# Kernel optimization log

Measured on AMD Instinct MI355X. Metric: run time of the kernel, lower is better.

Reference implementation:

```python
import jax, jax.numpy as jnp
import numpy as np

D_K = 64
D_MODEL = 1024
N_HEADS = 16


def setup_inputs() -> dict:
    key = jax.random.key(0)
    ks = jax.random.split(key, 9)
    B, S = 2, 2048
    scale = 1.0 / np.sqrt(D_MODEL)
    inp = {
        "x": jax.random.normal(ks[0], (B, S, D_MODEL), dtype=jnp.float32),
        "w_q": jax.random.normal(ks[1], (D_MODEL, N_HEADS * D_K), dtype=jnp.float32) * scale,
        "b_q": jnp.zeros((N_HEADS * D_K,), dtype=jnp.float32),
        "w_k": jax.random.normal(ks[2], (D_MODEL, N_HEADS * D_K), dtype=jnp.float32) * scale,
        "b_k": jnp.zeros((N_HEADS * D_K,), dtype=jnp.float32),
        "w_v": jax.random.normal(ks[3], (D_MODEL, N_HEADS * D_K), dtype=jnp.float32) * scale,
        "b_v": jnp.zeros((N_HEADS * D_K,), dtype=jnp.float32),
        "w_o": jax.random.normal(ks[4], (N_HEADS * D_K, D_MODEL), dtype=jnp.float32) * scale,
        "b_o": jnp.zeros((D_MODEL,), dtype=jnp.float32),
    }
    return inp


def reference(x, w_q, b_q, w_k, b_k, w_v, b_v, w_o, b_o):
    B, S, _ = x.shape
    H, Dk = N_HEADS, D_K

    def split_heads(m):  # [B,S,H*Dk] -> [B,H,S,Dk]
        return m.reshape(B, S, H, Dk).transpose(0, 2, 1, 3)

    Q = split_heads(x @ w_q + b_q)
    K = split_heads(x @ w_k + b_k)
    V = split_heads(x @ w_v + b_v)

    scores = jnp.einsum("bhsd,bhtd->bhst", Q, K) / jnp.sqrt(jnp.float32(Dk))
    probs = jax.nn.softmax(scores, axis=-1)
    attn = jnp.einsum("bhst,bhtd->bhsd", probs, V)  # [B,H,S,Dk]
    attn = attn.transpose(0, 2, 1, 3).reshape(B, S, H * Dk)
    return attn @ w_o + b_o
```

## Files before the change

### kernel.cpp

```cpp
#include <hip/hip_runtime.h>
#include <math.h>

#define D_MODELc 1024
#define N_HEADSc 16
#define D_Kc     64
#define B_SZc    2
#define S_LENc   2048
#define NTOKc    (B_SZc * S_LENc)

using half8  = __attribute__((ext_vector_type(8))) _Float16;
using half4  = __attribute__((ext_vector_type(4))) _Float16;
using float4v = __attribute__((ext_vector_type(4))) float;

__global__ __launch_bounds__(256) void cvt_all(
    const float* __restrict__ x,
    const float* __restrict__ W0, const float* __restrict__ W1,
    const float* __restrict__ W2, const float* __restrict__ W3,
    _Float16* __restrict__ wout, _Float16* __restrict__ xout)
{
    __shared__ float T[32][33];
    const int z = blockIdx.z;
    const int t = threadIdx.x;

    if (z == 4) {
        const int bid = blockIdx.y * 32 + blockIdx.x;
        #pragma unroll
        for (int c = 0; c < 2; ++c) {
            const int i = bid * 512 + c * 256 + t;
            float4v a = ((const float4v*)x)[2 * i];
            float4v b = ((const float4v*)x)[2 * i + 1];
            half8 h;
            h[0] = (_Float16)a[0]; h[1] = (_Float16)a[1];
            h[2] = (_Float16)a[2]; h[3] = (_Float16)a[3];
            h[4] = (_Float16)b[0]; h[5] = (_Float16)b[1];
            h[6] = (_Float16)b[2]; h[7] = (_Float16)b[3];
            ((half8*)xout)[i] = h;
        }
        return;
    }

    const float* W = (z == 0) ? W0 : (z == 1) ? W1 : (z == 2) ? W2 : W3;
    _Float16* O = wout + (size_t)z * 1024 * 1024;

    const int k0 = blockIdx.x * 32;
    const int n0 = blockIdx.y * 32;
    {
        const int r = t >> 3, c4 = (t & 7) * 4;
        float4v v = *(const float4v*)(W + (size_t)(k0 + r) * 1024 + n0 + c4);
        T[r][c4 + 0] = v[0]; T[r][c4 + 1] = v[1];
        T[r][c4 + 2] = v[2]; T[r][c4 + 3] = v[3];
    }
    __syncthreads();
    {
        const int rn = t >> 3, ck4 = (t & 7) * 4;
        half4 h;
        h[0] = (_Float16)T[ck4 + 0][rn];
        h[1] = (_Float16)T[ck4 + 1][rn];
        h[2] = (_Float16)T[ck4 + 2][rn];
        h[3] = (_Float16)T[ck4 + 3][rn];
        *(half4*)(O + (size_t)(n0 + rn) * 1024 + k0 + ck4) = h;
    }
}

template <int MODE>
__global__ __launch_bounds__(256) void gemm_f16(
    const _Float16* __restrict__ A, const _Float16* __restrict__ BtAll,
    const float* __restrict__ bias0, const float* __restrict__ bias1,
    const float* __restrict__ bias2, void* __restrict__ Cout)
{
    __shared__ _Float16 Als[128 * 32];
    __shared__ _Float16 Bls[128 * 32];

    constexpr int K = 1024;
    const int tid = threadIdx.x;
    const int m0  = blockIdx.x * 128;
    const int n0  = blockIdx.y * 128;
    const int z   = blockIdx.z;

    const _Float16* Bt  = BtAll + (size_t)z * 1024 * 1024;
    const float* bias   = (z == 0) ? bias0 : (z == 1) ? bias1 : bias2;
    const float qscale  = (MODE == 1 && z == 0) ? 0.18033688011112042f : 1.0f;

    const int wave = tid >> 6, lane = tid & 63;
    const int wr = wave >> 1, wc = wave & 1;
    const int quad = lane >> 4, l16 = lane & 15;

    float4v acc[4][4];
    #pragma unroll
    for (int i = 0; i < 4; ++i)
        #pragma unroll
        for (int j = 0; j < 4; ++j)
            acc[i][j] = (float4v){0.f, 0.f, 0.f, 0.f};

    for (int k0 = 0; k0 < K; k0 += 32) {
        #pragma unroll
        for (int c = 0; c < 2; ++c) {
            const int i   = c * 256 + tid;
            const int row = i >> 2, kc = i & 3;
            const _Float16* ga = A  + (size_t)(m0 + row) * K + k0 + kc * 8;
            const _Float16* gb = Bt + (size_t)(n0 + row) * K + k0 + kc * 8;
            __builtin_amdgcn_global_load_lds(
                (const __attribute__((address_space(1))) void*)ga,
                (__attribute__((address_space(3))) void*)(Als + i * 8), 16, 0, 0);
            __builtin_amdgcn_global_load_lds(
                (const __attribute__((address_space(1))) void*)gb,
                (__attribute__((address_space(3))) void*)(Bls + i * 8), 16, 0, 0);
        }
        __syncthreads();

        half8 af[4], bf[4];
        #pragma unroll
        for (int i = 0; i < 4; ++i) {
            const int r = wr * 64 + i * 16 + l16;
            af[i] = *(const half8*)(Als + r * 32 + quad * 8);
        }
        #pragma unroll
        for (int j = 0; j < 4; ++j) {
            const int cidx = wc * 64 + j * 16 + l16;
            bf[j] = *(const half8*)(Bls + cidx * 32 + quad * 8);
        }
        #pragma unroll
        for (int i = 0; i < 4; ++i)
            #pragma unroll
            for (int j = 0; j < 4; ++j)
                acc[i][j] = __builtin_amdgcn_mfma_f32_16x16x32_f16(
                    af[i], bf[j], acc[i][j], 0, 0, 0);
        __syncthreads();
    }

    if constexpr (MODE == 0) {
        #pragma unroll
        for (int i = 0; i < 4; ++i) {
            const int rbase = m0 + wr * 64 + i * 16 + quad * 4;
            #pragma unroll
            for (int j = 0; j < 4; ++j) {
                const int col = n0 + wc * 64 + j * 16 + l16;
                const float bv = bias[col];
                #pragma unroll
                for (int r = 0; r < 4; ++r)
                    ((float*)Cout)[(size_t)(rbase + r) * 1024 + col] =
                        acc[i][j][r] + bv;
            }
        }
    } else {
        if (z != 2) {
            #pragma unroll
            for (int i = 0; i < 4; ++i) {
                const int rbase = m0 + wr * 64 + i * 16 + quad * 4;
                #pragma unroll
                for (int j = 0; j < 4; ++j) {
                    const int col = n0 + wc * 64 + j * 16 + l16;
                    const float bv = bias[col];
                    #pragma unroll
                    for (int r = 0; r < 4; ++r) {
                        const float v = (acc[i][j][r] + bv) * qscale;
                        const int n = rbase + r;
                        const int b = n >> 11, s = n & 2047;
                        const int h = col >> 6, d = col & 63;
                        _Float16* C = (_Float16*)Cout + (size_t)z * NTOKc * D_MODELc;
                        C[(((size_t)(b * N_HEADSc + h)) * S_LENc + s) * D_Kc + d] =
                            (_Float16)v;
                    }
                }
            }
        } else {
            __shared__ _Float16 Tb[4 * 64 * 72];
            _Float16* tb = Tb + wave * (64 * 72);
            #pragma unroll
            for (int i = 0; i < 4; ++i) {
                #pragma unroll
                for (int j = 0; j < 4; ++j) {
                    const int col = n0 + wc * 64 + j * 16 + l16;
                    const float bv = bias[col];
                    half4 hv;
                    #pragma unroll
                    for (int r = 0; r < 4; ++r)
                        hv[r] = (_Float16)(acc[i][j][r] + bv);
                    *(half4*)(tb + (j * 16 + l16) * 72 + i * 16 + quad * 4) = hv;
                }
            }
            const int hh   = (n0 >> 6) + wc;
            const int tok0 = m0 + wr * 64;
            const int bb   = tok0 >> 11, sb = tok0 & 2047;
            const int dl   = lane >> 3, t8 = (lane & 7) * 8;
            _Float16* Vout = (_Float16*)Cout + (size_t)2 * NTOKc * D_MODELc;
            #pragma unroll
            for (int p = 0; p < 8; ++p) {
                const int d = p * 8 + dl;
                half8 hv = *(const half8*)(tb + d * 72 + t8);
                *(half8*)(Vout +
                    (((size_t)(bb * N_HEADSc + hh)) * D_Kc + d) * S_LENc +
                    sb + t8) = hv;
            }
        }
    }
}

__global__ __launch_bounds__(256) void attn_mfma(
    const _Float16* __restrict__ Qb, const _Float16* __restrict__ Kb,
    const _Float16* __restrict__ Vtg, _Float16* __restrict__ Ab)
{
    constexpr int PS = 72;
    __shared__ _Float16 Ks[64 * PS];
    __shared__ _Float16 Vt[64 * PS];
    __shared__ _Float16 Ps[128 * PS];
    __shared__ float    Al[128];

    const int tid  = threadIdx.x;
    const int wv   = tid >> 6;
    const int lane = tid & 63;
    const int quad = lane >> 4;
    const int l16  = lane & 15;

    const int q0 = blockIdx.x * 128;
    const int bh = blockIdx.y;
    const int b  = bh >> 4, h = bh & 15;

    const _Float16* Qsl = Qb  + (size_t)bh * S_LENc * D_Kc;
    const _Float16* Ksl = Kb  + (size_t)bh * S_LENc * D_Kc;
    const _Float16* Vsl = Vtg + (size_t)bh * S_LENc * D_Kc;

    half8 aq[2][2];
    #pragma unroll
    for (int qf = 0; qf < 2; ++qf) {
        const int row = q0 + wv * 32 + qf * 16 + l16;
        aq[qf][0] = *(const half8*)(Qsl + (size_t)row * 64 + quad * 8);
        aq[qf][1] = *(const half8*)(Qsl + (size_t)row * 64 + 32 + quad * 8);
    }

    float4v O[2][4];
    #pragma unroll
    for (int qf = 0; qf < 2; ++qf)
        #pragma unroll
        for (int nt = 0; nt < 4; ++nt)
            O[qf][nt] = (float4v){0.f, 0.f, 0.f, 0.f};
    float lr[2] = {0.f, 0.f};

    const int sr = tid >> 2;
    const int sg = (tid & 3) * 16;

    for (int t0 = 0; t0 < S_LENc; t0 += 64) {
        half8 k0 = *(const half8*)(Ksl + (size_t)(t0 + sr) * 64 + sg);
        half8 k1 = *(const half8*)(Ksl + (size_t)(t0 + sr) * 64 + sg + 8);
        half8 v0 = *(const half8*)(Vsl + (size_t)sr * S_LENc + t0 + sg);
        half8 v1 = *(const half8*)(Vsl + (size_t)sr * S_LENc + t0 + sg + 8);
        __syncthreads();
        *(half8*)(Ks + sr * PS + sg)     = k0;
        *(half8*)(Ks + sr * PS + sg + 8) = k1;
        *(half8*)(Vt + sr * PS + sg)     = v0;
        *(half8*)(Vt + sr * PS + sg + 8) = v1;
        __syncthreads();

        half8 kf[4][2];
        #pragma unroll
        for (int nt = 0; nt < 4; ++nt) {
            kf[nt][0] = *(const half8*)(Ks + (nt * 16 + l16) * PS + quad * 8);
            kf[nt][1] = *(const half8*)(Ks + (nt * 16 + l16) * PS + 32 + quad * 8);
        }

        #pragma unroll
        for (int qf = 0; qf < 2; ++qf) {
            float4v st[4];
            #pragma unroll
            for (int nt = 0; nt < 4; ++nt) {
                st[nt] = __builtin_amdgcn_mfma_f32_16x16x32_f16(
                    kf[nt][0], aq[qf][0], (float4v){0.f, 0.f, 0.f, 0.f}, 0, 0, 0);
                st[nt] = __builtin_amdgcn_mfma_f32_16x16x32_f16(
                    kf[nt][1], aq[qf][1], st[nt], 0, 0, 0);
            }
            float ls = 0.f;
            #pragma unroll
            for (int nt = 0; nt < 4; ++nt) {
                half4 pk;
                #pragma unroll
                for (int r = 0; r < 4; ++r) {
                    const float p = exp2f(fminf(st[nt][r], 15.5f));
                    ls += p;
                    pk[r] = (_Float16)p;
                }
                *(half4*)(Ps + (wv * 32 + qf * 16 + l16) * PS +
                          nt * 16 + quad * 4) = pk;
            }
            lr[qf] += ls;
        }

        half8 bvv[4][2];
        #pragma unroll
        for (int nt = 0; nt < 4; ++nt) {
            bvv[nt][0] = *(const half8*)(Vt + (nt * 16 + l16) * PS + quad * 8);
            bvv[nt][1] = *(const half8*)(Vt + (nt * 16 + l16) * PS + 32 + quad * 8);
        }
        #pragma unroll
        for (int qf = 0; qf < 2; ++qf) {
            half8 ap0 = *(const half8*)(Ps + (wv * 32 + qf * 16 + l16) * PS + quad * 8);
            half8 ap1 = *(const half8*)(Ps + (wv * 32 + qf * 16 + l16) * PS + 32 + quad * 8);
            #pragma unroll
            for (int nt = 0; nt < 4; ++nt) {
                O[qf][nt] = __builtin_amdgcn_mfma_f32_16x16x32_f16(
                    ap0, bvv[nt][0], O[qf][nt], 0, 0, 0);
                O[qf][nt] = __builtin_amdgcn_mfma_f32_16x16x32_f16(
                    ap1, bvv[nt][1], O[qf][nt], 0, 0, 0);
            }
        }
    }

    #pragma unroll
    for (int qf = 0; qf < 2; ++qf) {
        float t = lr[qf];
        t += __shfl_xor(t, 16, 64);
        t += __shfl_xor(t, 32, 64);
        if (quad == 0) Al[wv * 32 + qf * 16 + l16] = 1.0f / t;
    }
    #pragma unroll
    for (int qf = 0; qf < 2; ++qf) {
        float4v iv = *(const float4v*)(Al + wv * 32 + qf * 16 + quad * 4);
        #pragma unroll
        for (int r = 0; r < 4; ++r) {
            const int q = q0 + wv * 32 + qf * 16 + quad * 4 + r;
            _Float16* dst = Ab + ((size_t)(b * S_LENc + q)) * 1024 + h * 64;
            #pragma unroll
            for (int nt = 0; nt < 4; ++nt)
                dst[nt * 16 + l16] = (_Float16)(O[qf][nt][r] * iv[r]);
        }
    }
}

extern "C" void kernel_launch(void* const* d_in, const int* in_sizes, int n_in,
                              void* d_out, int out_size, void* d_ws, size_t ws_size,
                              hipStream_t stream)
{
    const float* x  = (const float*)d_in[0];
    const float* wq = (const float*)d_in[1];
    const float* bq = (const float*)d_in[2];
    const float* wk = (const float*)d_in[3];
    const float* bk = (const float*)d_in[4];
    const float* wv = (const float*)d_in[5];
    const float* bv = (const float*)d_in[6];
    const float* wo = (const float*)d_in[7];
    const float* bo = (const float*)d_in[8];
    float* out = (float*)d_out;

    const size_t M1 = 1024 * 1024;
    const size_t M4 = 4 * M1;
    _Float16* xh = (_Float16*)d_ws;
    _Float16* wh = xh + M4;
    _Float16* Qh = wh + M4;
    _Float16* Ah = Qh + 3 * M4;

    cvt_all<<<dim3(32, 32, 5), dim3(256), 0, stream>>>(
        x, wq, wk, wv, wo, wh, xh);
    gemm_f16<1><<<dim3(NTOKc / 128, D_MODELc / 128, 3), dim3(256), 0, stream>>>(
        xh, wh, bq, bk, bv, Qh);
    attn_mfma<<<dim3(S_LENc / 128, B_SZc * N_HEADSc), dim3(256), 0, stream>>>(
        Qh, Qh + M4, Qh + 2 * M4, Ah);
    gemm_f16<0><<<dim3(NTOKc / 128, D_MODELc / 128, 1), dim3(256), 0, stream>>>(
        Ah, wh + 3 * M1, bo, bo, bo, out);
}
```

Baseline: 216.6 us.

## Split attention over key halves with a combine kernel, simplify V store

```diff
diff --git a/kernel.cpp b/kernel.cpp
--- a/kernel.cpp
+++ b/kernel.cpp
@@ -10,6 +10,7 @@
 
 using half8  = __attribute__((ext_vector_type(8))) _Float16;
 using half4  = __attribute__((ext_vector_type(4))) _Float16;
+using fp16x2 = __attribute__((ext_vector_type(2))) __fp16;
 using float4v = __attribute__((ext_vector_type(4))) float;
 
 __global__ __launch_bounds__(256) void cvt_all(
@@ -164,33 +165,23 @@
                 }
             }
         } else {
-            __shared__ _Float16 Tb[4 * 64 * 72];
-            _Float16* tb = Tb + wave * (64 * 72);
             #pragma unroll
             for (int i = 0; i < 4; ++i) {
+                const int rbase = m0 + wr * 64 + i * 16 + quad * 4;
+                const int b = rbase >> 11, s0 = rbase & 2047;
                 #pragma unroll
                 for (int j = 0; j < 4; ++j) {
                     const int col = n0 + wc * 64 + j * 16 + l16;
                     const float bv = bias[col];
+                    const int h = col >> 6, d = col & 63;
                     half4 hv;
                     #pragma unroll
                     for (int r = 0; r < 4; ++r)
                         hv[r] = (_Float16)(acc[i][j][r] + bv);
-                    *(half4*)(tb + (j * 16 + l16) * 72 + i * 16 + quad * 4) = hv;
+                    _Float16* C = (_Float16*)Cout + (size_t)2 * NTOKc * D_MODELc;
+                    *(half4*)(C + (((size_t)(b * N_HEADSc + h)) * D_Kc + d) *
+                              S_LENc + s0) = hv;
                 }
-            }
-            const int hh   = (n0 >> 6) + wc;
-            const int tok0 = m0 + wr * 64;
-            const int bb   = tok0 >> 11, sb = tok0 & 2047;
-            const int dl   = lane >> 3, t8 = (lane & 7) * 8;
-            _Float16* Vout = (_Float16*)Cout + (size_t)2 * NTOKc * D_MODELc;
-            #pragma unroll
-            for (int p = 0; p < 8; ++p) {
-                const int d = p * 8 + dl;
-                half8 hv = *(const half8*)(tb + d * 72 + t8);
-                *(half8*)(Vout +
-                    (((size_t)(bb * N_HEADSc + hh)) * D_Kc + d) * S_LENc +
-                    sb + t8) = hv;
             }
         }
     }
@@ -198,13 +189,13 @@
 
 __global__ __launch_bounds__(256) void attn_mfma(
     const _Float16* __restrict__ Qb, const _Float16* __restrict__ Kb,
-    const _Float16* __restrict__ Vtg, _Float16* __restrict__ Ab)
+    const _Float16* __restrict__ Vtg, _Float16* __restrict__ Op,
+    float* __restrict__ Lp)
 {
     constexpr int PS = 72;
     __shared__ _Float16 Ks[64 * PS];
     __shared__ _Float16 Vt[64 * PS];
     __shared__ _Float16 Ps[128 * PS];
-    __shared__ float    Al[128];
 
     const int tid  = threadIdx.x;
     const int wv   = tid >> 6;
@@ -214,7 +205,8 @@
 
     const int q0 = blockIdx.x * 128;
     const int bh = blockIdx.y;
-    const int b  = bh >> 4, h = bh & 15;
+    const int sp = blockIdx.z;
+    const int kb = sp * (S_LENc / 2);
 
     const _Float16* Qsl = Qb  + (size_t)bh * S_LENc * D_Kc;
     const _Float16* Ksl = Kb  + (size_t)bh * S_LENc * D_Kc;
@@ -239,7 +231,7 @@
     const int sr = tid >> 2;
     const int sg = (tid & 3) * 16;
 
-    for (int t0 = 0; t0 < S_LENc; t0 += 64) {
+    for (int t0 = kb; t0 < kb + S_LENc / 2; t0 += 64) {
         half8 k0 = *(const half8*)(Ksl + (size_t)(t0 + sr) * 64 + sg);
         half8 k1 = *(const half8*)(Ksl + (size_t)(t0 + sr) * 64 + sg + 8);
         half8 v0 = *(const half8*)(Vsl + (size_t)sr * S_LENc + t0 + sg);
@@ -271,15 +263,16 @@
             float ls = 0.f;
             #pragma unroll
             for (int nt = 0; nt < 4; ++nt) {
-                half4 pk;
-                #pragma unroll
-                for (int r = 0; r < 4; ++r) {
-                    const float p = exp2f(fminf(st[nt][r], 15.5f));
-                    ls += p;
-                    pk[r] = (_Float16)p;
-                }
+                const float p0 = __builtin_amdgcn_exp2f(fminf(st[nt][0], 15.5f));
+                const float p1 = __builtin_amdgcn_exp2f(fminf(st[nt][1], 15.5f));
+                const float p2 = __builtin_amdgcn_exp2f(fminf(st[nt][2], 15.5f));
+                const float p3 = __builtin_amdgcn_exp2f(fminf(st[nt][3], 15.5f));
+                ls += (p0 + p1) + (p2 + p3);
+                union { fp16x2 h2[2]; half4 h4; } u;
+                u.h2[0] = __builtin_amdgcn_cvt_pkrtz(p0, p1);
+                u.h2[1] = __builtin_amdgcn_cvt_pkrtz(p2, p3);
                 *(half4*)(Ps + (wv * 32 + qf * 16 + l16) * PS +
-                          nt * 16 + quad * 4) = pk;
+                          nt * 16 + quad * 4) = u.h4;
             }
             lr[qf] += ls;
         }
@@ -304,25 +297,44 @@
         }
     }
 
+    const size_t qgb = (size_t)bh * S_LENc;
     #pragma unroll
     for (int qf = 0; qf < 2; ++qf) {
         float t = lr[qf];
         t += __shfl_xor(t, 16, 64);
         t += __shfl_xor(t, 32, 64);
-        if (quad == 0) Al[wv * 32 + qf * 16 + l16] = 1.0f / t;
-    }
-    #pragma unroll
-    for (int qf = 0; qf < 2; ++qf) {
-        float4v iv = *(const float4v*)(Al + wv * 32 + qf * 16 + quad * 4);
+        if (quad == 0)
+            Lp[(size_t)sp * 65536 + qgb + q0 + wv * 32 + qf * 16 + l16] = t;
         #pragma unroll
         for (int r = 0; r < 4; ++r) {
             const int q = q0 + wv * 32 + qf * 16 + quad * 4 + r;
-            _Float16* dst = Ab + ((size_t)(b * S_LENc + q)) * 1024 + h * 64;
+            _Float16* dst = Op + ((size_t)sp * 65536 + qgb + q) * 64;
             #pragma unroll
             for (int nt = 0; nt < 4; ++nt)
-                dst[nt * 16 + l16] = (_Float16)(O[qf][nt][r] * iv[r]);
-        }
-    }
+                dst[nt * 16 + l16] = (_Float16)O[qf][nt][r];
+        }
+    }
+}
+
+__global__ __launch_bounds__(256) void attn_combine(
+    const _Float16* __restrict__ Op, const float* __restrict__ Lp,
+    _Float16* __restrict__ Ab)
+{
+    const int i  = blockIdx.x * 256 + threadIdx.x;
+    const int e0 = i * 8;
+    const int qg = e0 >> 6;
+    const int d0 = e0 & 63;
+    const int bh = qg >> 11, q = qg & 2047;
+    const int b  = bh >> 4,  h = bh & 15;
+
+    const float inv = 1.0f / (Lp[qg] + Lp[65536 + qg]);
+    half8 o0 = *(const half8*)(Op + (size_t)qg * 64 + d0);
+    half8 o1 = *(const half8*)(Op + ((size_t)65536 + qg) * 64 + d0);
+    half8 hv;
+    #pragma unroll
+    for (int j = 0; j < 8; ++j)
+        hv[j] = (_Float16)(((float)o0[j] + (float)o1[j]) * inv);
+    *(half8*)(Ab + ((size_t)(b * S_LENc + q)) * 1024 + h * 64 + d0) = hv;
 }
 
 extern "C" void kernel_launch(void* const* d_in, const int* in_sizes, int n_in,
@@ -345,14 +357,18 @@
     _Float16* xh = (_Float16*)d_ws;
     _Float16* wh = xh + M4;
     _Float16* Qh = wh + M4;
-    _Float16* Ah = Qh + 3 * M4;
+    _Float16* Oph = Qh + 3 * M4;
+    float*    Lp  = (float*)(Oph + 2 * M4);
+    _Float16* Ah = xh;
 
     cvt_all<<<dim3(32, 32, 5), dim3(256), 0, stream>>>(
         x, wq, wk, wv, wo, wh, xh);
     gemm_f16<1><<<dim3(NTOKc / 128, D_MODELc / 128, 3), dim3(256), 0, stream>>>(
         xh, wh, bq, bk, bv, Qh);
-    attn_mfma<<<dim3(S_LENc / 128, B_SZc * N_HEADSc), dim3(256), 0, stream>>>(
-        Qh, Qh + M4, Qh + 2 * M4, Ah);
+    attn_mfma<<<dim3(S_LENc / 128, B_SZc * N_HEADSc, 2), dim3(256), 0, stream>>>(
+        Qh, Qh + M4, Qh + 2 * M4, Oph, Lp);
+    attn_combine<<<dim3(NTOKc * D_MODELc / 8 / 256), dim3(256), 0, stream>>>(
+        Oph, Lp, Ah);
     gemm_f16<0><<<dim3(NTOKc / 128, D_MODELc / 128, 1), dim3(256), 0, stream>>>(
         Ah, wh + 3 * M1, bo, bo, bo, out);
 }
```

Result: no change. 218.9 us (+1.1%).
